# Optimization experiments

Measured on AMD Instinct MI355X. Metric: run time of the kernel, lower is better.

Reference implementation:

```python
import jax, jax.numpy as jnp
import numpy as np

EPS = 1e-6  # floor

def setup_inputs() -> dict:
    key = jax.random.key(0)
    k1, = jax.random.split(key, 1)
    # mel-spectrogram magnitudes: non-negative
    x = jax.random.uniform(k1, (64, 2048, 160, 1), dtype=jnp.float32)  # [B,T,F,C]
    alpha = jnp.array([0.98], dtype=jnp.float32)
    smooth = jnp.array([0.03], dtype=jnp.float32)
    delta = jnp.array([2.0], dtype=jnp.float32)
    root = jnp.array([0.5], dtype=jnp.float32)
    return {"x": x, "alpha": alpha, "smooth": smooth, "delta": delta, "root": root}

def reference(x, alpha, smooth, delta, root):
    # EMA recurrence over time: m[t] = (1 - s) * x[t] + s * m[t-1], m[-1] = 0
    xt = jnp.swapaxes(x, 0, 1)  # [T,B,F,C]

    def step(prev, cur):
        new = (1.0 - smooth) * cur + smooth * prev
        return new, new

    _, smoothed_t = jax.lax.scan(step, jnp.zeros_like(xt[0]), xt)
    smoothed = jnp.swapaxes(smoothed_t, 0, 1)  # [B,T,F,C]

    # PCEN: (x / (eps + M)^alpha + delta)^root - delta^root
    pcen = (x / (EPS + smoothed) ** alpha + delta) ** root - delta ** root
    return pcen
```

## Files before the change

### kernel.cpp

```cpp
#include <hip/hip_runtime.h>
#include <stdint.h>

#define EPS 1e-6f

constexpr int Bq   = 64;
constexpr int Tq   = 2048;
constexpr int Fq   = 160;
constexpr int FQ4  = 40;
constexpr int ROWS = 64;
constexpr int WARM = 8;
constexpr int CH   = 8;
constexpr int TPB  = 320;
constexpr int NTILE = Tq / ROWS;
constexpr int NWG   = Bq * NTILE;

typedef float f4 __attribute__((ext_vector_type(4)));

__device__ __forceinline__ float fast_pow_pos(float b, float e) {
    return __builtin_amdgcn_exp2f(e * __builtin_amdgcn_logf(b));
}

template<bool RSQ>
__device__ __forceinline__ float pcen_one(float xv, float h, float na, float oms,
                                          float r, float d, float droot) {
    float me    = fmaf(oms, h, EPS);
    float ratio = xv * __builtin_amdgcn_exp2f(na * __builtin_amdgcn_logf(me));
    if (RSQ) return __builtin_amdgcn_sqrtf(ratio + d) - droot;
    else     return fast_pow_pos(ratio + d, r) - droot;
}

__device__ __forceinline__ void ema4(f4& h, const f4 xv, float s) {
    h.x = fmaf(s, h.x, xv.x);
    h.y = fmaf(s, h.y, xv.y);
    h.z = fmaf(s, h.z, xv.z);
    h.w = fmaf(s, h.w, xv.w);
}

template<bool RSQ>
__device__ __forceinline__ void main_loop(const f4 (&xm)[CH], f4 h,
                                          float s, float oms, float na,
                                          float r, float d, float droot,
                                          f4* __restrict__ outr, int gbase) {
#pragma unroll
    for (int j = 0; j < CH; ++j) {
        ema4(h, xm[j], s);
        f4 o;
        o.x = pcen_one<RSQ>(xm[j].x, h.x, na, oms, r, d, droot);
        o.y = pcen_one<RSQ>(xm[j].y, h.y, na, oms, r, d, droot);
        o.z = pcen_one<RSQ>(xm[j].z, h.z, na, oms, r, d, droot);
        o.w = pcen_one<RSQ>(xm[j].w, h.w, na, oms, r, d, droot);
        __builtin_nontemporal_store(o, &outr[gbase + j * FQ4]);
    }
}

__global__ __launch_bounds__(TPB) void pcen_kernel(
    const float* __restrict__ x,
    const float* __restrict__ alpha_p,
    const float* __restrict__ smooth_p,
    const float* __restrict__ delta_p,
    const float* __restrict__ root_p,
    float* __restrict__ out)
{
    const int wg    = ((blockIdx.x & 7) << 8) | (blockIdx.x >> 3);
    const int tile  = wg % NTILE;
    const int b     = wg / NTILE;
    const int r0    = b * Tq + tile * ROWS;

    const int f = threadIdx.x % FQ4;
    const int c = threadIdx.x / FQ4;

    const float* tb = x + (size_t)(r0 + c * CH) * Fq + f * 4;
    const bool haswarm = !(tile == 0 && c == 0);

    f4 xw[WARM];
    if (haswarm) {
#pragma unroll
        for (int j = 0; j < WARM; ++j)
            xw[j] = *(const f4*)(tb + (j - WARM) * Fq);
    }
    f4 xm[CH];
#pragma unroll
    for (int j = 0; j < CH; ++j)
        xm[j] = *(const f4*)(tb + j * Fq);

    const float s     = smooth_p[0];
    const float a     = alpha_p[0];
    const float d     = delta_p[0];
    const float r     = root_p[0];
    const float oms   = 1.0f - s;
    const float na    = -a;
    const bool  rsq   = (r == 0.5f);
    const float droot = rsq ? __builtin_amdgcn_sqrtf(d) : fast_pow_pos(d, r);

    f4 h = (f4){0.f, 0.f, 0.f, 0.f};
    if (haswarm) {
#pragma unroll
        for (int j = 0; j < WARM; ++j)
            ema4(h, xw[j], s);
    }

    f4* __restrict__ outr = (f4*)out;
    const int gbase = (r0 + c * CH) * FQ4 + f;

    if (rsq) main_loop<true >(xm, h, s, oms, na, r, d, droot, outr, gbase);
    else     main_loop<false>(xm, h, s, oms, na, r, d, droot, outr, gbase);
}

extern "C" void kernel_launch(void* const* d_in, const int* in_sizes, int n_in,
                              void* d_out, int out_size, void* d_ws, size_t ws_size,
                              hipStream_t stream) {
    const float* x      = (const float*)d_in[0];
    const float* alpha  = (const float*)d_in[1];
    const float* smooth = (const float*)d_in[2];
    const float* delta  = (const float*)d_in[3];
    const float* root   = (const float*)d_in[4];
    float* out          = (float*)d_out;

    pcen_kernel<<<NWG, TPB, 0, stream>>>(x, alpha, smooth, delta, root, out);
}
```

Baseline: 159.1 us.

## Use persistent blocks with double-buffered register prefetch across work items

Replaces the one-tile-per-block launch with a fixed grid of 512 blocks where each thread slot processes several (batch, tile, chunk) items. The next item's warmup and main loads are issued into a second register buffer before computing the current one, with scheduling barriers to keep the loads ahead. This aims to hide global load latency and reduce block launch overhead, at the cost of doubled register buffers and fewer resident waves.

```diff
diff --git a/kernel.cpp b/kernel.cpp
--- a/kernel.cpp
+++ b/kernel.cpp
@@ -12,7 +12,11 @@
 constexpr int CH   = 8;
 constexpr int TPB  = 320;
 constexpr int NTILE = Tq / ROWS;
-constexpr int NWG   = Bq * NTILE;
+constexpr int NITEM = Bq * NTILE * (ROWS / CH);
+constexpr int BLKS  = 512;
+constexpr int SLOTS = TPB / FQ4;
+constexpr int NQ    = BLKS * SLOTS;
+constexpr int ITEMS = NITEM / NQ;
 
 typedef float f4 __attribute__((ext_vector_type(4)));
 
@@ -37,23 +41,68 @@
 }
 
 template<bool RSQ>
-__device__ __forceinline__ void main_loop(const f4 (&xm)[CH], f4 h,
-                                          float s, float oms, float na,
-                                          float r, float d, float droot,
-                                          f4* __restrict__ outr, int gbase) {
+__device__ __forceinline__ void run(const float* __restrict__ x,
+                                    float* __restrict__ out,
+                                    int q, int f,
+                                    float s, float oms, float na,
+                                    float r, float d, float droot)
+{
+    f4* __restrict__ outr = (f4*)out;
+
+    f4 wA[WARM], mA[CH]; int r0A; bool hwA;
+    f4 wB[WARM], mB[CH]; int r0B; bool hwB;
+
+    auto issue = [&](int W, f4 (&xw)[WARM], f4 (&xm)[CH], int& r0, bool& hw) {
+        const int c    = W & (SLOTS - 1);
+        const int tile = (W >> 3) & (NTILE - 1);
+        const int b    = W >> 8;
+        r0 = b * Tq + tile * ROWS + c * CH;
+        hw = ((W & 255) != 0);
+        const float* tb = x + (size_t)r0 * Fq + f * 4;
+        const float* wb = hw ? tb - WARM * Fq : tb;
 #pragma unroll
-    for (int j = 0; j < CH; ++j) {
-        ema4(h, xm[j], s);
-        f4 o;
-        o.x = pcen_one<RSQ>(xm[j].x, h.x, na, oms, r, d, droot);
-        o.y = pcen_one<RSQ>(xm[j].y, h.y, na, oms, r, d, droot);
-        o.z = pcen_one<RSQ>(xm[j].z, h.z, na, oms, r, d, droot);
-        o.w = pcen_one<RSQ>(xm[j].w, h.w, na, oms, r, d, droot);
-        __builtin_nontemporal_store(o, &outr[gbase + j * FQ4]);
+        for (int j = 0; j < WARM; ++j) xw[j] = *(const f4*)(wb + j * Fq);
+#pragma unroll
+        for (int j = 0; j < CH; ++j)   xm[j] = *(const f4*)(tb + j * Fq);
+    };
+
+    auto compute = [&](const f4 (&xw)[WARM], const f4 (&xm)[CH], int r0, bool hw) {
+        f4 h = (f4){0.f, 0.f, 0.f, 0.f};
+        if (hw) {
+#pragma unroll
+            for (int j = 0; j < WARM; ++j) ema4(h, xw[j], s);
+        }
+        const int gb = r0 * FQ4 + f;
+#pragma unroll
+        for (int j = 0; j < CH; ++j) {
+            ema4(h, xm[j], s);
+            f4 o;
+            o.x = pcen_one<RSQ>(xm[j].x, h.x, na, oms, r, d, droot);
+            o.y = pcen_one<RSQ>(xm[j].y, h.y, na, oms, r, d, droot);
+            o.z = pcen_one<RSQ>(xm[j].z, h.z, na, oms, r, d, droot);
+            o.w = pcen_one<RSQ>(xm[j].w, h.w, na, oms, r, d, droot);
+            __builtin_nontemporal_store(o, &outr[gb + j * FQ4]);
+        }
+    };
+
+    issue(q, wA, mA, r0A, hwA);
+    __builtin_amdgcn_sched_barrier(0);
+
+#pragma unroll
+    for (int k = 0; k < ITEMS; ++k) {
+        if ((k & 1) == 0) {
+            if (k + 1 < ITEMS) issue(q + (k + 1) * NQ, wB, mB, r0B, hwB);
+            __builtin_amdgcn_sched_barrier(0);
+            compute(wA, mA, r0A, hwA);
+        } else {
+            if (k + 1 < ITEMS) issue(q + (k + 1) * NQ, wA, mA, r0A, hwA);
+            __builtin_amdgcn_sched_barrier(0);
+            compute(wB, mB, r0B, hwB);
+        }
     }
 }
 
-__global__ __launch_bounds__(TPB) void pcen_kernel(
+__global__ __launch_bounds__(TPB, 3) void pcen_kernel(
     const float* __restrict__ x,
     const float* __restrict__ alpha_p,
     const float* __restrict__ smooth_p,
@@ -61,27 +110,10 @@
     const float* __restrict__ root_p,
     float* __restrict__ out)
 {
-    const int wg    = ((blockIdx.x & 7) << 8) | (blockIdx.x >> 3);
-    const int tile  = wg % NTILE;
-    const int b     = wg / NTILE;
-    const int r0    = b * Tq + tile * ROWS;
-
-    const int f = threadIdx.x % FQ4;
-    const int c = threadIdx.x / FQ4;
-
-    const float* tb = x + (size_t)(r0 + c * CH) * Fq + f * 4;
-    const bool haswarm = !(tile == 0 && c == 0);
-
-    f4 xw[WARM];
-    if (haswarm) {
-#pragma unroll
-        for (int j = 0; j < WARM; ++j)
-            xw[j] = *(const f4*)(tb + (j - WARM) * Fq);
-    }
-    f4 xm[CH];
-#pragma unroll
-    for (int j = 0; j < CH; ++j)
-        xm[j] = *(const f4*)(tb + j * Fq);
+    const int bid  = ((blockIdx.x & 7) << 6) | (blockIdx.x >> 3);
+    const int f    = threadIdx.x % FQ4;
+    const int slot = threadIdx.x / FQ4;
+    const int q    = bid * SLOTS + slot;
 
     const float s     = smooth_p[0];
     const float a     = alpha_p[0];
@@ -92,18 +124,8 @@
     const bool  rsq   = (r == 0.5f);
     const float droot = rsq ? __builtin_amdgcn_sqrtf(d) : fast_pow_pos(d, r);
 
-    f4 h = (f4){0.f, 0.f, 0.f, 0.f};
-    if (haswarm) {
-#pragma unroll
-        for (int j = 0; j < WARM; ++j)
-            ema4(h, xw[j], s);
-    }
-
-    f4* __restrict__ outr = (f4*)out;
-    const int gbase = (r0 + c * CH) * FQ4 + f;
-
-    if (rsq) main_loop<true >(xm, h, s, oms, na, r, d, droot, outr, gbase);
-    else     main_loop<false>(xm, h, s, oms, na, r, d, droot, outr, gbase);
+    if (rsq) run<true >(x, out, q, f, s, oms, na, r, d, droot);
+    else     run<false>(x, out, q, f, s, oms, na, r, d, droot);
 }
 
 extern "C" void kernel_launch(void* const* d_in, const int* in_sizes, int n_in,
@@ -116,5 +138,5 @@
     const float* root   = (const float*)d_in[4];
     float* out          = (float*)d_out;
 
-    pcen_kernel<<<NWG, TPB, 0, stream>>>(x, alpha, smooth, delta, root, out);
+    pcen_kernel<<<BLKS, TPB, 0, stream>>>(x, alpha, smooth, delta, root, out);
 }
```

Result: no change. 160.4 us (+0.8%).
